# Optimization experiments

Measured on AMD Instinct MI355X. Metric: run time of the kernel, lower is better.

The kernel has to match this reference:

```python
import jax, jax.numpy as jnp
import numpy as np

IN_CH = 1280
NUM_HEADS = 8
DIM_DOWN = 5
CUT_RATE = 4
SCALE = (IN_CH // NUM_HEADS) ** -0.5  # faithful to original: uses in_ch//num_heads


def setup_inputs() -> dict:
    key = jax.random.key(0)
    ks = jax.random.split(key, 5)
    B, N = 4, 4096
    C = IN_CH // DIM_DOWN  # 256
    x = jax.random.normal(ks[0], (B, N, IN_CH), dtype=jnp.float32)
    Wd = jax.random.normal(ks[1], (IN_CH, C), dtype=jnp.float32) * (IN_CH ** -0.5)
    Wqkv = jax.random.normal(ks[2], (C, 3 * C), dtype=jnp.float32) * (C ** -0.5)
    Wup = jax.random.normal(ks[3], (C, IN_CH), dtype=jnp.float32) * (C ** -0.5)
    bup = jnp.zeros((IN_CH,), dtype=jnp.float32)
    return {"x": x, "Wd": Wd, "Wqkv": Wqkv, "Wup": Wup, "bup": bup}


def reference(x, Wd, Wqkv, Wup, bup):
    # dim-down projection (dropout is identity at rate 0 / eval)
    h = x @ Wd                                  # [B, N, C]
    B, N, C = h.shape
    H = NUM_HEADS
    hd = C // H
    blk = N // CUT_RATE
    qkv = (h @ Wqkv).reshape(B, N, 3, H, hd)
    qkv = jnp.transpose(qkv, (2, 0, 3, 1, 4))   # [3, B, H, N, hd]
    q, k, v = qkv[0], qkv[1], qkv[2]
    # block-diagonal local attention: split N into CUT_RATE independent chunks
    q = q.reshape(B, H, CUT_RATE, blk, hd)
    k = k.reshape(B, H, CUT_RATE, blk, hd)
    v = v.reshape(B, H, CUT_RATE, blk, hd)
    attn = jnp.einsum('bhcqd,bhckd->bhcqk', q, k) * SCALE
    attn = jax.nn.softmax(attn, axis=-1)
    o = jnp.einsum('bhcqk,bhckd->bhcqd', attn, v)
    # torch cat over chunks along token dim, then merge heads: [B, N, C]
    o = jnp.transpose(o, (0, 2, 3, 1, 4)).reshape(B, N, C)
    return o @ Wup + bup
```

## Files before the change

kernel.cpp:

```cpp
#include <hip/hip_runtime.h>

typedef unsigned short u16;
typedef unsigned int u32;
typedef u16 u16x4 __attribute__((ext_vector_type(4)));
typedef u16 u16x8 __attribute__((ext_vector_type(8)));
typedef __bf16 bf16x8 __attribute__((ext_vector_type(8)));
typedef float f32x4 __attribute__((ext_vector_type(4)));

__device__ __forceinline__ u16 f2bf(float f) {
  union { float f; unsigned u; } c; c.f = f;
  unsigned u = c.u;
  return (u16)((u + 0x7fff + ((u >> 16) & 1)) >> 16);
}

__device__ __forceinline__ float fexp2(float x) {
  float r; asm("v_exp_f32 %0, %1" : "=v"(r) : "v"(x)); return r;
}

__device__ __forceinline__ u32 cvtpk(float lo, float hi) {
  u32 r;
  asm("v_cvt_pk_bf16_f32 %0, %1, %2" : "=v"(r) : "v"(lo), "v"(hi));
  return r;
}

__device__ __forceinline__ void lds16(const u16* g, u16* l) {
  __builtin_amdgcn_global_load_lds(
      (const __attribute__((address_space(1))) unsigned int*)g,
      (__attribute__((address_space(3))) unsigned int*)l, 16, 0, 0);
}

#define CEXP (0.07905694150420949f * 1.4426950408889634f)

#define BAR()  do { asm volatile("" ::: "memory"); \
                    __builtin_amdgcn_s_barrier(); \
                    asm volatile("" ::: "memory"); } while (0)
#define VMC(n) asm volatile("s_waitcnt vmcnt(" #n ")" ::: "memory")

#define PREP_W (1280 * 256 + 768 * 256 + 1280 * 256)

__global__ __launch_bounds__(256)
void prep_all(const float* __restrict__ Wd, const float* __restrict__ Wqkv,
              const float* __restrict__ Wup, const float* __restrict__ X,
              u16* __restrict__ WdC, u16* __restrict__ WqkvT,
              u16* __restrict__ WupT, u16* __restrict__ Xb, int n8) {
  int id = blockIdx.x * 256 + threadIdx.x;
  if (id < 1280 * 256) {
    WdC[id] = f2bf(Wd[id]);
    return;
  }
  id -= 1280 * 256;
  if (id < 768 * 256) {
    int n = id >> 8, c = id & 255;
    float v = Wqkv[(size_t)c * 768 + n];
    if (n < 256) v *= CEXP;
    WqkvT[id] = f2bf(v);
    return;
  }
  id -= 768 * 256;
  if (id < 1280 * 256) {
    int n = id >> 8, c = id & 255;
    WupT[id] = f2bf(Wup[(size_t)c * 1280 + n]);
    return;
  }
  id -= 1280 * 256;
  if (id < n8) {
    const float4* src = (const float4*)(X + (size_t)id * 8);
    float4 lo = src[0], hi = src[1];
    u16x8 v;
    v[0]=f2bf(lo.x); v[1]=f2bf(lo.y); v[2]=f2bf(lo.z); v[3]=f2bf(lo.w);
    v[4]=f2bf(hi.x); v[5]=f2bf(hi.y); v[6]=f2bf(hi.z); v[7]=f2bf(hi.w);
    *(u16x8*)(Xb + (size_t)id * 8) = v;
  }
}

template <int AF32>
__global__ __launch_bounds__(256)
void gemm_bt(const void* __restrict__ Av,
             const u16* __restrict__ BT,
             u16* __restrict__ Cb, float* __restrict__ Cf,
             const float* __restrict__ bias,
             int M, int N, int K)
{
  __shared__ u16 As[128][64];
  __shared__ u16 Bs[128][64];
  const int tid  = threadIdx.x;
  const int wave = tid >> 6, lane = tid & 63;
  const int quad = lane >> 4, l16 = lane & 15;
  const int rsw  = l16 & 7;
  const int ssw  = ((lane & 7) ^ (lane >> 3)) << 3;

  const int nb = N >> 7, mb = M >> 7;
  int band, nblk;
  if ((mb & 7) == 0) {
    int xcd = blockIdx.x & 7, slot = blockIdx.x >> 3;
    band = xcd + 8 * (slot / nb);
    nblk = slot % nb;
  } else {
    band = blockIdx.x / nb;
    nblk = blockIdx.x % nb;
  }
  const int m0 = band * 128, n0 = nblk * 128;
  const int wr = (wave >> 1) * 64, wc = (wave & 1) * 64;
  const u16*   A16 = (const u16*)Av;
  const float* A32 = (const float*)Av;

  f32x4 acc[4][4];
#pragma unroll
  for (int i = 0; i < 4; i++)
#pragma unroll
    for (int j = 0; j < 4; j++) acc[i][j] = f32x4{0.f, 0.f, 0.f, 0.f};

  for (int k0 = 0; k0 < K; k0 += 64) {
    if constexpr (AF32) {
#pragma unroll
      for (int it = 0; it < 4; it++) {
        int idx = tid + it * 256;
        int r = idx >> 3;
        const float* src = &A32[(size_t)(m0 + r) * K + k0 + ((idx & 7) << 3)];
        float4 lo = *(const float4*)src;
        float4 hi = *(const float4*)(src + 4);
        u16x8 v;
        v[0]=f2bf(lo.x); v[1]=f2bf(lo.y); v[2]=f2bf(lo.z); v[3]=f2bf(lo.w);
        v[4]=f2bf(hi.x); v[5]=f2bf(hi.y); v[6]=f2bf(hi.z); v[7]=f2bf(hi.w);
        *(u16x8*)&As[r][((idx & 7) ^ (r & 7)) << 3] = v;
      }
#pragma unroll
      for (int it = 0; it < 4; it++) {
        int r0 = wave * 32 + it * 8;
        lds16(&BT[(size_t)(n0 + r0 + (lane >> 3)) * K + k0 + ssw],
              &Bs[r0][0] + lane * 8);
      }
    } else {
#pragma unroll
      for (int it = 0; it < 4; it++) {
        int r0 = wave * 32 + it * 8;
        lds16(&A16[(size_t)(m0 + r0 + (lane >> 3)) * K + k0 + ssw],
              &As[r0][0] + lane * 8);
        lds16(&BT[(size_t)(n0 + r0 + (lane >> 3)) * K + k0 + ssw],
              &Bs[r0][0] + lane * 8);
      }
    }
    __syncthreads();
#pragma unroll
    for (int ks = 0; ks < 64; ks += 32) {
      bf16x8 af[4], bfr[4];
#pragma unroll
      for (int i = 0; i < 4; i++)
        af[i] = *(const bf16x8*)&As[wr + i * 16 + l16][(((ks >> 3) + quad) ^ rsw) << 3];
#pragma unroll
      for (int j = 0; j < 4; j++)
        bfr[j] = *(const bf16x8*)&Bs[wc + j * 16 + l16][(((ks >> 3) + quad) ^ rsw) << 3];
#pragma unroll
      for (int i = 0; i < 4; i++)
#pragma unroll
        for (int j = 0; j < 4; j++)
          acc[i][j] = __builtin_amdgcn_mfma_f32_16x16x32_bf16(af[i], bfr[j], acc[i][j], 0, 0, 0);
    }
    __syncthreads();
  }

#pragma unroll
  for (int i = 0; i < 4; i++) {
#pragma unroll
    for (int j = 0; j < 4; j++) {
      int col = n0 + wc + j * 16 + l16;
      float bv = bias ? bias[col] : 0.0f;
#pragma unroll
      for (int r = 0; r < 4; r++) {
        int row = m0 + wr + i * 16 + quad * 4 + r;
        float v = acc[i][j][r] + bv;
        if (Cf) Cf[(size_t)row * N + col] = v;
        else    Cb[(size_t)row * N + col] = f2bf(v);
      }
    }
  }
}

#define LDA_(d, ib) { _Pragma("unroll") for (int i = 0; i < 4; i++) \
  _Pragma("unroll") for (int ks = 0; ks < 2; ks++) \
    af[i*2+ks] = *(const bf16x8*)&As[d][wm][(ib+i)*16 + l16][((ks*4+quad) ^ rsw) << 3]; }

#define LDB_(d, dst, jp) { _Pragma("unroll") for (int j = 0; j < 2; j++) \
  _Pragma("unroll") for (int ks = 0; ks < 2; ks++) \
    dst[j*2+ks] = *(const bf16x8*)&Bs[d][bh][br + (jp*2+j)*16 + l16][((ks*4+quad) ^ rsw) << 3]; }

#define MM_(ib, jp, breg) { __builtin_amdgcn_s_setprio(1); \
  _Pragma("unroll") for (int i = 0; i < 4; i++) \
  _Pragma("unroll") for (int j = 0; j < 2; j++) \
  _Pragma("unroll") for (int ks = 0; ks < 2; ks++) \
    acc[ib+i][jp*2+j] = __builtin_amdgcn_mfma_f32_16x16x32_bf16( \
        af[i*2+ks], breg[j*2+ks], acc[ib+i][jp*2+j], 0, 0, 0); \
  __builtin_amdgcn_s_setprio(0); }

template <int F32OUT>
__global__ __launch_bounds__(512, 2)
void gemm_bt256(const u16* __restrict__ A16, const u16* __restrict__ BT,
                u16* __restrict__ Cb, float* __restrict__ Cf,
                const float* __restrict__ bias, int M, int N, int K)
{
  __shared__ __align__(16) u16 As[2][2][128][64];
  __shared__ __align__(16) u16 Bs[2][2][128][64];
  const int tid  = threadIdx.x;
  const int wave = tid >> 6, lane = tid & 63;
  const int quad = lane >> 4, l16 = lane & 15;
  const int wm = wave >> 2, wn = wave & 3;
  const int bh = wn >> 1, br = (wn & 1) * 64;
  const int rsw = l16 & 7;

  const int nb = N >> 8, mb = M >> 8;
  int band, nblk;
  if ((mb & 7) == 0) {
    int xcd = blockIdx.x & 7, slot = blockIdx.x >> 3;
    band = xcd + 8 * (slot / nb);
    nblk = slot % nb;
  } else {
    band = blockIdx.x / nb;
    nblk = blockIdx.x % nb;
  }
  const int m0 = band * 256, n0 = nblk * 256;
  const int NT = K >> 6;

  const int srow = tid >> 3;
  const int scol = ((tid & 7) ^ (srow & 7)) << 3;

  auto stageA = [&](int t, int h) {
    const int d = t & 1;
    const size_t g = (size_t)(m0 + h * 128 + srow) * K + (t << 6) + scol;
    lds16(&A16[g], &As[d][h][0][0] + tid * 8);
    lds16(&A16[g + (size_t)64 * K], &As[d][h][64][0] + tid * 8);
  };
  auto stageB = [&](int t, int h) {
    const int d = t & 1;
    const size_t g = (size_t)(n0 + h * 128 + srow) * K + (t << 6) + scol;
    lds16(&BT[g], &Bs[d][h][0][0] + tid * 8);
    lds16(&BT[g + (size_t)64 * K], &Bs[d][h][64][0] + tid * 8);
  };

  bf16x8 af[8], b0[4], b1[4];
  f32x4 acc[8][4];
#pragma unroll
  for (int i = 0; i < 8; i++)
#pragma unroll
    for (int j = 0; j < 4; j++) acc[i][j] = f32x4{0.f, 0.f, 0.f, 0.f};

  stageA(0, 0); stageA(0, 1); stageB(0, 0); stageB(0, 1); stageA(1, 0);
  VMC(2);
  BAR();

  const int nIter = NT >> 1;
  for (int it = 0; it < nIter; ++it) {
    const int t0 = it * 2, t1 = t0 + 1;
    const bool more  = (t0 + 2 < NT);
    const bool more1 = (t1 + 2 < NT);

    LDA_(0, 0); LDB_(0, b0, 0);
    stageA(t1, 1);
    BAR(); MM_(0, 0, b0); BAR();
    LDB_(0, b1, 1);
    stageB(t1, 0);
    BAR(); MM_(0, 1, b1); BAR();
    LDA_(0, 4);
    stageB(t1, 1);
    BAR(); MM_(4, 1, b1); BAR();
    if (more) stageA(t0 + 2, 0);
    BAR(); MM_(4, 0, b0);
    if (more) { VMC(2); } else { VMC(0); }
    BAR();

    LDA_(1, 0); LDB_(1, b0, 0);
    if (more) stageA(t0 + 2, 1);
    BAR(); MM_(0, 0, b0); BAR();
    LDB_(1, b1, 1);
    if (more) stageB(t0 + 2, 0);
    BAR(); MM_(0, 1, b1); BAR();
    LDA_(1, 4);
    if (more) stageB(t0 + 2, 1);
    BAR(); MM_(4, 1, b1); BAR();
    if (more1) stageA(t1 + 2, 0);
    BAR(); MM_(4, 0, b0);
    if (it + 1 < nIter) {
      if (more1) { VMC(2); } else { VMC(0); }
      BAR();
    }
  }

#pragma unroll
  for (int i = 0; i < 8; i++) {
#pragma unroll
    for (int j = 0; j < 4; j++) {
      const int col = n0 + wn * 64 + j * 16 + l16;
      float bv = F32OUT ? bias[col] : 0.0f;
#pragma unroll
      for (int r = 0; r < 4; r++) {
        const int row = m0 + wm * 128 + i * 16 + quad * 4 + r;
        if constexpr (F32OUT) Cf[(size_t)row * N + col] = acc[i][j][r] + bv;
        else                  Cb[(size_t)row * N + col] = f2bf(acc[i][j][r]);
      }
    }
  }
}

__global__ __launch_bounds__(256)
void vtrans(const u16* __restrict__ qkv, u16* __restrict__ vT)
{
  __shared__ u16 T[32][72];
  const int tid   = threadIdx.x;
  const int kt    = blockIdx.x;
  const int head  = blockIdx.y >> 2;
  const int chunk = blockIdx.y & 3;
  const int b     = blockIdx.z;
  const size_t rowbase = (size_t)b * 4096 + chunk * 1024 + kt * 64;

  const int tok = tid >> 2;
  const int d8  = (tid & 3) << 3;
  u16x8 vv = *(const u16x8*)&qkv[(rowbase + tok) * 768 + 512 + head * 32 + d8];
  const int rot = (tok + (d8 >> 3)) & 7;
#pragma unroll
  for (int jj = 0; jj < 8; jj++) {
    int j = (jj + rot) & 7;
    T[d8 + j][tok] = vv[j];
  }
  __syncthreads();
  const int d = tid >> 3;
  const int s = tid & 7;
  const int base = ((s >> 2) << 5) + ((s & 3) << 2);
  u16x4 lo = *(const u16x4*)&T[d][base];
  u16x4 hi = *(const u16x4*)&T[d][base + 16];
  u16x8 o8;
  o8[0]=lo[0]; o8[1]=lo[1]; o8[2]=lo[2]; o8[3]=lo[3];
  o8[4]=hi[0]; o8[5]=hi[1]; o8[6]=hi[2]; o8[7]=hi[3];
  size_t obase = ((size_t)((b * 4 + chunk) * 8 + head)) * 32768
               + (size_t)d * 1024 + kt * 64 + s * 8;
  *(u16x8*)&vT[obase] = o8;
}

__global__ __launch_bounds__(256)
void attn_kernel(const u16* __restrict__ qkv, const u16* __restrict__ vT,
                 u16* __restrict__ o)
{
  __shared__ __align__(16) u16 Ks[4][64][32];
  __shared__ __align__(16) u16 VTs[4][32][64];

  const int tid  = threadIdx.x;
  const int wave = tid >> 6, lane = tid & 63;
  const int quad = lane >> 4, l16 = lane & 15;
  const int qb    = blockIdx.x;
  const int head  = blockIdx.y >> 2;
  const int chunk = blockIdx.y & 3;
  const int b     = blockIdx.z;
  const size_t rowbase = (size_t)b * 4096 + chunk * 1024;
  const int tok0 = qb * 128 + wave * 32;

  const int kkey = tid >> 2;
  const int kd8  = (tid & 3) << 3;
  const int vr   = tid >> 3;
  const int vs   = tid & 7;
  const int vsl  = (vs ^ (vr & 7)) << 3;
  const size_t vbase = ((size_t)((b * 4 + chunk) * 8 + head)) * 32768
                     + (size_t)vr * 1024 + vsl;

  auto stageKV = [&](int kb, int buf) {
    lds16(&qkv[(rowbase + kb * 64 + kkey) * 768 + 256 + head * 32 + kd8],
          &Ks[buf][0][0] + tid * 8);
    lds16(&vT[vbase + (size_t)kb * 64], &VTs[buf][0][0] + tid * 8);
  };

  stageKV(0, 0);

  bf16x8 qf[2];
#pragma unroll
  for (int qt = 0; qt < 2; qt++)
    qf[qt] = *(const bf16x8*)&qkv[(rowbase + tok0 + qt * 16 + l16) * 768 + head * 32 + quad * 8];

  stageKV(1, 1);

  float lsum[2] = {0.f, 0.f};
  f32x4 Oacc[2][2];
#pragma unroll
  for (int qt = 0; qt < 2; qt++)
#pragma unroll
    for (int nd = 0; nd < 2; nd++) Oacc[qt][nd] = f32x4{0.f, 0.f, 0.f, 0.f};

  VMC(2);
  BAR();

  for (int kb = 0; kb < 16; kb++) {
    const int cur = kb & 3;
    if (kb + 2 < 16) stageKV(kb + 2, (kb + 2) & 3);

    bf16x8 kf[4];
#pragma unroll
    for (int kt = 0; kt < 4; kt++)
      kf[kt] = *(const bf16x8*)&Ks[cur][kt * 16 + l16][quad * 8];

    f32x4 ST[4][2];
    __builtin_amdgcn_s_setprio(1);
#pragma unroll
    for (int kt = 0; kt < 4; kt++)
#pragma unroll
      for (int qt = 0; qt < 2; qt++)
        ST[kt][qt] = __builtin_amdgcn_mfma_f32_16x16x32_bf16(kf[kt], qf[qt], f32x4{0.f,0.f,0.f,0.f}, 0, 0, 0);
    __builtin_amdgcn_s_setprio(0);

    u32 pw[2][4][2];
#pragma unroll
    for (int qt = 0; qt < 2; qt++)
#pragma unroll
      for (int kt = 0; kt < 4; kt++) {
        float p0 = fexp2(ST[kt][qt][0]);
        float p1 = fexp2(ST[kt][qt][1]);
        float p2 = fexp2(ST[kt][qt][2]);
        float p3 = fexp2(ST[kt][qt][3]);
        lsum[qt] += (p0 + p1) + (p2 + p3);
        pw[qt][kt][0] = cvtpk(p0, p1);
        pw[qt][kt][1] = cvtpk(p2, p3);
      }

#pragma unroll
    for (int ks = 0; ks < 2; ks++) {
      bf16x8 vf[2];
#pragma unroll
      for (int nd = 0; nd < 2; nd++)
        vf[nd] = *(const bf16x8*)&VTs[cur][nd * 16 + l16][((ks * 4 + quad) ^ (l16 & 7)) << 3];
      __builtin_amdgcn_s_setprio(1);
#pragma unroll
      for (int qt = 0; qt < 2; qt++) {
        union { u32 w[4]; bf16x8 v; } pu;
        pu.w[0] = pw[qt][2 * ks][0];
        pu.w[1] = pw[qt][2 * ks][1];
        pu.w[2] = pw[qt][2 * ks + 1][0];
        pu.w[3] = pw[qt][2 * ks + 1][1];
#pragma unroll
        for (int nd = 0; nd < 2; nd++)
          Oacc[qt][nd] = __builtin_amdgcn_mfma_f32_16x16x32_bf16(pu.v, vf[nd], Oacc[qt][nd], 0, 0, 0);
      }
      __builtin_amdgcn_s_setprio(0);
    }

    if (kb < 15) {
      if (kb + 2 < 16) { VMC(2); } else { VMC(0); }
      BAR();
    }
  }

#pragma unroll
  for (int qt = 0; qt < 2; qt++) {
    float s = lsum[qt];
    s += __shfl_xor(s, 16);
    s += __shfl_xor(s, 32);
    lsum[qt] = s;
  }
#pragma unroll
  for (int qt = 0; qt < 2; qt++)
#pragma unroll
    for (int r = 0; r < 4; r++) {
      float inv = 1.0f / __shfl(lsum[qt], quad * 4 + r, 16);
      size_t row = rowbase + tok0 + qt * 16 + quad * 4 + r;
#pragma unroll
      for (int nd = 0; nd < 2; nd++) {
        int col = head * 32 + nd * 16 + l16;
        o[row * 256 + col] = f2bf(Oacc[qt][nd][r] * inv);
      }
    }
}

extern "C" void kernel_launch(void* const* d_in, const int* in_sizes, int n_in,
                              void* d_out, int out_size, void* d_ws, size_t ws_size,
                              hipStream_t stream)
{
  const float* x    = (const float*)d_in[0];
  const float* Wd   = (const float*)d_in[1];
  const float* Wqkv = (const float*)d_in[2];
  const float* Wup  = (const float*)d_in[3];
  const float* bup  = (const float*)d_in[4];
  float* out = (float*)d_out;

  const int M = 4 * 4096;

  u16* WdC   = (u16*)d_ws;
  u16* WqkvT = WdC   + 1280 * 256;
  u16* WupT  = WqkvT + 768 * 256;
  u16* WpT   = WupT  + 1280 * 256;
  u16* qkv   = WpT   + 768 * 1280;
  u16* ob    = qkv   + (size_t)M * 768;
  u16* xb    = ob    + (size_t)M * 256;
  u16* vT    = xb;

  const size_t need = ((size_t)(1280*256 + 768*256 + 1280*256 + 768*1280)
                       + (size_t)M * (768 + 256 + 1280)) * sizeof(u16);
  const bool use_xb = ws_size >= need;

  const int n8 = use_xb ? (M * 1280 / 8) : 0;
  prep_all<<<(PREP_W + n8 + 255) / 256, 256, 0, stream>>>(
      Wd, Wqkv, Wup, x, WdC, WqkvT, WupT, xb, n8);

  gemm_bt<0><<<dim3((1280 / 128) * (768 / 128)), 256, 0, stream>>>(
      (const void*)WqkvT, WdC, WpT, nullptr, nullptr, 768, 1280, 256);

  if (use_xb) {
    gemm_bt256<0><<<dim3((768 / 256) * (M / 256)), 512, 0, stream>>>(
        xb, WpT, qkv, nullptr, nullptr, M, 768, 1280);
  } else {
    gemm_bt<1><<<dim3((768 / 128) * (M / 128)), 256, 0, stream>>>(
        (const void*)x, WpT, qkv, nullptr, nullptr, M, 768, 1280);
  }

  vtrans<<<dim3(16, 32, 4), 256, 0, stream>>>(qkv, vT);

  attn_kernel<<<dim3(8, 32, 4), 256, 0, stream>>>(qkv, vT, ob);

  gemm_bt256<1><<<dim3((1280 / 256) * (M / 256)), 512, 0, stream>>>(
      ob, WupT, nullptr, out, bup, M, 1280, 256);
}
```

Measured before the change: 277.7 us.

## Compute softmax row sums via MFMA with ones and use 128-tile GEMM for up-projection

In attention, the per-row exp-sum is no longer accumulated with VALU adds and cross-lane shuffles. An extra MFMA multiplies the bf16 probability tile by a vector of ones, so the row sums land directly in accumulator layout. This also makes the sums consistent with the bf16-rounded probabilities. Separately, the final up-projection GEMM (K=256, fp32 output with bias) switches from the 256x256-tile kernel to the 128x128-tile gemm_bt, aiming for more blocks and better occupancy on the short-K GEMM, and gemm_bt256 drops its fp32 template path.

```diff
diff --git a/kernel.cpp b/kernel.cpp
--- a/kernel.cpp
+++ b/kernel.cpp
@@ -192,11 +192,9 @@
         af[i*2+ks], breg[j*2+ks], acc[ib+i][jp*2+j], 0, 0, 0); \
   __builtin_amdgcn_s_setprio(0); }
 
-template <int F32OUT>
 __global__ __launch_bounds__(512, 2)
 void gemm_bt256(const u16* __restrict__ A16, const u16* __restrict__ BT,
-                u16* __restrict__ Cb, float* __restrict__ Cf,
-                const float* __restrict__ bias, int M, int N, int K)
+                u16* __restrict__ Cb, int M, int N, int K)
 {
   __shared__ __align__(16) u16 As[2][2][128][64];
   __shared__ __align__(16) u16 Bs[2][2][128][64];
@@ -289,12 +287,10 @@
 #pragma unroll
     for (int j = 0; j < 4; j++) {
       const int col = n0 + wn * 64 + j * 16 + l16;
-      float bv = F32OUT ? bias[col] : 0.0f;
 #pragma unroll
       for (int r = 0; r < 4; r++) {
         const int row = m0 + wm * 128 + i * 16 + quad * 4 + r;
-        if constexpr (F32OUT) Cf[(size_t)row * N + col] = acc[i][j][r] + bv;
-        else                  Cb[(size_t)row * N + col] = f2bf(acc[i][j][r]);
+        Cb[(size_t)row * N + col] = f2bf(acc[i][j][r]);
       }
     }
   }
@@ -374,12 +370,21 @@
 
   stageKV(1, 1);
 
-  float lsum[2] = {0.f, 0.f};
-  f32x4 Oacc[2][2];
-#pragma unroll
-  for (int qt = 0; qt < 2; qt++)
+  bf16x8 onesb;
+  {
+    union { u16x8 u; bf16x8 v; } c;
+#pragma unroll
+    for (int i = 0; i < 8; i++) c.u[i] = 0x3F80;
+    onesb = c.v;
+  }
+
+  f32x4 Oacc[2][2], Osum[2];
+#pragma unroll
+  for (int qt = 0; qt < 2; qt++) {
+    Osum[qt] = f32x4{0.f, 0.f, 0.f, 0.f};
 #pragma unroll
     for (int nd = 0; nd < 2; nd++) Oacc[qt][nd] = f32x4{0.f, 0.f, 0.f, 0.f};
+  }
 
   VMC(2);
   BAR();
@@ -411,7 +416,6 @@
         float p1 = fexp2(ST[kt][qt][1]);
         float p2 = fexp2(ST[kt][qt][2]);
         float p3 = fexp2(ST[kt][qt][3]);
-        lsum[qt] += (p0 + p1) + (p2 + p3);
         pw[qt][kt][0] = cvtpk(p0, p1);
         pw[qt][kt][1] = cvtpk(p2, p3);
       }
@@ -433,6 +437,7 @@
 #pragma unroll
         for (int nd = 0; nd < 2; nd++)
           Oacc[qt][nd] = __builtin_amdgcn_mfma_f32_16x16x32_bf16(pu.v, vf[nd], Oacc[qt][nd], 0, 0, 0);
+        Osum[qt] = __builtin_amdgcn_mfma_f32_16x16x32_bf16(pu.v, onesb, Osum[qt], 0, 0, 0);
       }
       __builtin_amdgcn_s_setprio(0);
     }
@@ -444,17 +449,10 @@
   }
 
 #pragma unroll
-  for (int qt = 0; qt < 2; qt++) {
-    float s = lsum[qt];
-    s += __shfl_xor(s, 16);
-    s += __shfl_xor(s, 32);
-    lsum[qt] = s;
-  }
-#pragma unroll
   for (int qt = 0; qt < 2; qt++)
 #pragma unroll
     for (int r = 0; r < 4; r++) {
-      float inv = 1.0f / __shfl(lsum[qt], quad * 4 + r, 16);
+      float inv = 1.0f / Osum[qt][r];
       size_t row = rowbase + tok0 + qt * 16 + quad * 4 + r;
 #pragma unroll
       for (int nd = 0; nd < 2; nd++) {
@@ -498,8 +496,8 @@
       (const void*)WqkvT, WdC, WpT, nullptr, nullptr, 768, 1280, 256);
 
   if (use_xb) {
-    gemm_bt256<0><<<dim3((768 / 256) * (M / 256)), 512, 0, stream>>>(
-        xb, WpT, qkv, nullptr, nullptr, M, 768, 1280);
+    gemm_bt256<<<dim3((768 / 256) * (M / 256)), 512, 0, stream>>>(
+        xb, WpT, qkv, M, 768, 1280);
   } else {
     gemm_bt<1><<<dim3((768 / 128) * (M / 128)), 256, 0, stream>>>(
         (const void*)x, WpT, qkv, nullptr, nullptr, M, 768, 1280);
@@ -509,6 +507,6 @@
 
   attn_kernel<<<dim3(8, 32, 4), 256, 0, stream>>>(qkv, vT, ob);
 
-  gemm_bt256<1><<<dim3((1280 / 256) * (M / 256)), 512, 0, stream>>>(
-      ob, WupT, nullptr, out, bup, M, 1280, 256);
-}
+  gemm_bt<0><<<dim3((1280 / 128) * (M / 128)), 256, 0, stream>>>(
+      (const void*)ob, WupT, nullptr, out, bup, M, 1280, 256);
+}
```

After: 273.9 us. No clear change (-1.4%).
